# Kernel tuning notes

Hardware: AMD Instinct MI355X
Metric: run time of the kernel (lower is better)

## Reference

```python
import jax, jax.numpy as jnp
import numpy as np

B, L, S, D, H = 32, 256, 64, 128, 4
DH = D // H
EPS = 1e-5


def _uniform(k, shape, scale):
    return jax.random.uniform(k, shape, jnp.float32, -scale, scale)


def setup_inputs() -> dict:
    key = jax.random.key(0)
    ks = jax.random.split(key, 12)
    sc = 1.0 / np.sqrt(D)
    return {
        "h_wq": jax.random.normal(ks[0], (B, L, D), jnp.float32),
        "h_all": jax.random.normal(ks[1], (B, L, S, D), jnp.float32),
        "station_id": jax.random.randint(ks[2], (B,), 0, S),
        "adj": jax.random.randint(ks[3], (S, S), 0, 2).astype(jnp.float32),
        "in_proj_w": _uniform(ks[4], (3 * D, D), sc),
        "in_proj_b": _uniform(ks[5], (3 * D,), sc),
        "out_w": _uniform(ks[6], (D, D), sc),
        "out_b": _uniform(ks[7], (D,), sc),
        "gate_w": _uniform(ks[8], (D, 2 * D), 1.0 / np.sqrt(2 * D)),
        "gate_b": _uniform(ks[9], (D,), 1.0 / np.sqrt(2 * D)),
        "ln_g": jnp.ones((D,), jnp.float32),
        "ln_b": jnp.zeros((D,), jnp.float32),
        "alpha": jnp.asarray(0.1, jnp.float32),
    }


def _allowed_mask(adj, station_id):
    # allowed[b, s] == True  <=> station s may attend as key for sample b
    sid = station_id.astype(jnp.int32)
    allowed = adj[sid] > 0.0                                  # [B, S]
    self_oh = jax.nn.one_hot(sid, adj.shape[0], dtype=bool)   # [B, S]
    allowed = allowed & ~self_oh                              # exclude self
    # fallback-to-all for rows with no neighbor (still excluding self)
    no_nb = ~jnp.any(allowed, axis=1, keepdims=True)
    allowed = jnp.where(no_nb, ~self_oh, allowed)
    # final safety: if STILL empty (S==1 edge case), allow self
    no_nb2 = ~jnp.any(allowed, axis=1, keepdims=True)
    allowed = allowed | (no_nb2 & self_oh)
    return allowed


def _forward(h_wq, h_all, station_id, adj, in_proj_w, in_proj_b,
             out_w, out_b, gate_w, gate_b, ln_g, ln_b, alpha):
    b, l, d = h_wq.shape
    s = h_all.shape[2]
    qw, kw, vw = jnp.split(in_proj_w, 3, axis=0)
    qb, kb, vb = jnp.split(in_proj_b, 3, axis=0)

    q = (h_wq @ qw.T + qb).reshape(b, l, H, DH)        # [B,L,H,DH]
    k = (h_all @ kw.T + kb).reshape(b, l, s, H, DH)    # [B,L,S,H,DH]
    v = (h_all @ vw.T + vb).reshape(b, l, s, H, DH)

    scores = jnp.einsum('blhd,blshd->blhs', q, k) / np.sqrt(DH)  # [B,L,H,S]
    allowed = _allowed_mask(adj, station_id)                     # [B,S]
    scores = jnp.where(allowed[:, None, None, :], scores, -jnp.inf)
    w = jax.nn.softmax(scores, axis=-1)

    ctx = jnp.einsum('blhs,blshd->blhd', w, v).reshape(b, l, d)
    ctx = ctx @ out_w.T + out_b                                  # out_proj

    g = jax.nn.sigmoid(jnp.concatenate([h_wq, ctx], axis=-1) @ gate_w.T + gate_b)
    y = h_wq + alpha * (g * ctx)                                 # dropout = eval mode

    mu = jnp.mean(y, axis=-1, keepdims=True)
    var = jnp.mean(jnp.square(y - mu), axis=-1, keepdims=True)
    return (y - mu) * jax.lax.rsqrt(var + EPS) * ln_g + ln_b


def reference(h_wq, h_all, station_id, adj, in_proj_w, in_proj_b,
              out_w, out_b, gate_w, gate_b, ln_g, ln_b, alpha):
    return _forward(h_wq, h_all, station_id, adj, in_proj_w, in_proj_b,
                    out_w, out_b, gate_w, gate_b, ln_g, ln_b, alpha)
```

## Files before the change

### kernel.cpp

```cpp
#include <hip/hip_runtime.h>
#include <math.h>

#define B_   32
#define L_   256
#define S_   64
#define D_   128
#define H_   4
#define DH_  32
#define NTOK (B_*L_)

#define QK_OFF   0
#define QK_BYTES ((size_t)NTOK*512*4)
#define CB_OFF   (QK_OFF + QK_BYTES)
#define CB_BYTES ((size_t)NTOK*4*4)
#define CTX_OFF  (CB_OFF + CB_BYTES)

__global__ __launch_bounds__(256) void qk_kernel(
        const float* __restrict__ h_wq,
        const float* __restrict__ in_proj_w, const float* __restrict__ in_proj_b,
        float* __restrict__ qk_out, float* __restrict__ cb_out) {
    __shared__ float x_lds[32*128];
    __shared__ float q_lds[32*128];
    const int t0 = blockIdx.x * 32;
    const int tid = threadIdx.x;

    {
        const float4* src = (const float4*)(h_wq + (size_t)t0*128);
        float4* dst = (float4*)x_lds;
        for (int e = tid; e < 32*32; e += 256) dst[e] = src[e];
    }
    __syncthreads();

    const int d = tid & 127, half = tid >> 7;
    const float* xb = x_lds + half*16*128;
    {
        float acc[16];
        const float qb = in_proj_b[d];
        #pragma unroll
        for (int t = 0; t < 16; ++t) acc[t] = qb;
        const float4* wrow = (const float4*)(in_proj_w + (size_t)d*128);
        for (int j4 = 0; j4 < 32; ++j4) {
            float4 w = wrow[j4];
            #pragma unroll
            for (int t = 0; t < 16; ++t) {
                float4 x = *(const float4*)(xb + t*128 + j4*4);
                acc[t] += w.x*x.x + w.y*x.y + w.z*x.z + w.w*x.w;
            }
        }
        #pragma unroll
        for (int t = 0; t < 16; ++t) q_lds[(half*16+t)*128 + d] = acc[t];
    }
    __syncthreads();

    const float scale = 0.17677669529663687f;
    const float* qbse = q_lds + half*16*128;
    #pragma unroll
    for (int h = 0; h < 4; ++h) {
        float acc[16];
        #pragma unroll
        for (int t = 0; t < 16; ++t) acc[t] = 0.f;
        for (int j = 0; j < 32; ++j) {
            float w = in_proj_w[(size_t)(128 + h*32 + j)*128 + d];
            #pragma unroll
            for (int t = 0; t < 16; ++t) acc[t] += w * qbse[t*128 + h*32 + j];
        }
        #pragma unroll
        for (int t = 0; t < 16; ++t)
            qk_out[(size_t)(t0 + half*16 + t)*512 + h*128 + d] = acc[t] * scale;
    }
    if (tid < 128) {
        int t = tid >> 2, h = tid & 3;
        float s = 0.f;
        for (int j = 0; j < 32; ++j)
            s += q_lds[t*128 + h*32 + j] * in_proj_b[128 + h*32 + j];
        cb_out[(t0 + t)*4 + h] = s * scale;
    }
}

__global__ __launch_bounds__(256) void attn_kernel(
        const float* __restrict__ h_all,
        const float* __restrict__ in_proj_w, const float* __restrict__ in_proj_b,
        const float* __restrict__ qk_buf, const float* __restrict__ cb_buf,
        const int* __restrict__ station_id, const float* __restrict__ adj,
        float* __restrict__ ctx_out) {
    __shared__ float u_lds[4][4*132];
    __shared__ int   lst[64];
    __shared__ int   cnt_s;

    const int t0  = blockIdx.x * 4;
    const int b   = t0 >> 8;
    const int tid = threadIdx.x;
    const int wv  = tid >> 6;
    const int lane = tid & 63;
    const int g   = lane >> 4;
    const int lg  = lane & 15;
    const int t = t0 + wv;

    if (tid < 64) {
        int sid = station_id[b];
        int s = tid;
        bool av = (adj[sid*S_ + s] > 0.0f) && (s != sid);
        unsigned long long m = __ballot(av);
        if (m == 0ull) { av = (s != sid); m = __ballot(av); }
        if (m == 0ull) { av = (s == sid); m = __ballot(av); }
        int idx = __popcll(m & ((1ull << s) - 1ull));
        if (av) lst[idx] = s;
        if (s == 0) cnt_s = __popcll(m);
    }

    const float* qkp = qk_buf + (size_t)t*512 + g*128 + 8*lg;
    const float4 qa = *(const float4*)(qkp);
    const float4 qb = *(const float4*)(qkp + 4);
    const float cbg = cb_buf[t*4 + g];

    __syncthreads();
    const int cnt = cnt_s;
    const float* rowbase = h_all + (size_t)t * (S_*D_) + 8*lg;

    float mg = -INFINITY, lsum = 0.f;
    float4 ua = {0.f,0.f,0.f,0.f}, ub = {0.f,0.f,0.f,0.f};

    #pragma unroll 2
    for (int i = 0; i < cnt; ++i) {
        const float* rp = rowbase + lst[i]*D_;
        float4 xa = *(const float4*)(rp);
        float4 xb = *(const float4*)(rp + 4);
        float p = qa.x*xa.x + qa.y*xa.y + qa.z*xa.z + qa.w*xa.w
                + qb.x*xb.x + qb.y*xb.y + qb.z*xb.z + qb.w*xb.w;
        p += __shfl_xor(p, 8, 16);
        p += __shfl_xor(p, 4, 16);
        p += __shfl_xor(p, 2, 16);
        p += __shfl_xor(p, 1, 16);
        float s = p + cbg;
        float n = fmaxf(mg, s);
        float r = __expf(mg - n), w = __expf(s - n);
        lsum = lsum*r + w;
        ua.x = ua.x*r + w*xa.x; ua.y = ua.y*r + w*xa.y;
        ua.z = ua.z*r + w*xa.z; ua.w = ua.w*r + w*xa.w;
        ub.x = ub.x*r + w*xb.x; ub.y = ub.y*r + w*xb.y;
        ub.z = ub.z*r + w*xb.z; ub.w = ub.w*r + w*xb.w;
        mg = n;
    }
    {
        float inv = 1.f / lsum;
        ua.x *= inv; ua.y *= inv; ua.z *= inv; ua.w *= inv;
        ub.x *= inv; ub.y *= inv; ub.z *= inv; ub.w *= inv;
        *(float4*)&u_lds[wv][g*132 + 8*lg]     = ua;
        *(float4*)&u_lds[wv][g*132 + 8*lg + 4] = ub;
    }
    __syncthreads();

    {
        const int d = tid & 127, pr = tid >> 7, h = (tid & 127) >> 5;
        const float4* vwrow = (const float4*)(in_proj_w + (size_t)(256 + d)*128);
        const float vb = in_proj_b[256 + d];
        float a0 = vb, a1 = vb;
        const float* uA = &u_lds[2*pr][h*132];
        const float* uB = &u_lds[2*pr+1][h*132];
        #pragma unroll 8
        for (int j4 = 0; j4 < 32; ++j4) {
            float4 w = vwrow[j4];
            float4 v0 = *(const float4*)(uA + j4*4);
            float4 v1 = *(const float4*)(uB + j4*4);
            a0 += w.x*v0.x + w.y*v0.y + w.z*v0.z + w.w*v0.w;
            a1 += w.x*v1.x + w.y*v1.y + w.z*v1.z + w.w*v1.w;
        }
        ctx_out[(size_t)(t0 + 2*pr    )*128 + d] = a0;
        ctx_out[(size_t)(t0 + 2*pr + 1)*128 + d] = a1;
    }
}

__global__ __launch_bounds__(256) void epi_kernel(
        const float* __restrict__ h_wq, const float* __restrict__ ctx_buf,
        const float* __restrict__ out_w, const float* __restrict__ out_b,
        const float* __restrict__ gate_w, const float* __restrict__ gate_b,
        const float* __restrict__ ln_g, const float* __restrict__ ln_b,
        const float* __restrict__ alpha, float* __restrict__ out) {
    __shared__ float c_tile[32*128];
    __shared__ float x_tile[32*128];
    __shared__ float o_tile[32*128];
    __shared__ float mu_s[32], rs_s[32];
    const int t0 = blockIdx.x * 32;
    const int tid = threadIdx.x;

    {
        const float4* cs = (const float4*)(ctx_buf + (size_t)t0*128);
        const float4* xs = (const float4*)(h_wq + (size_t)t0*128);
        float4* cd = (float4*)c_tile; float4* xd = (float4*)x_tile;
        for (int e = tid; e < 32*32; e += 256) { cd[e] = cs[e]; xd[e] = xs[e]; }
    }
    __syncthreads();

    const int d = tid & 127, half = tid >> 7;
    float o_acc[16];
    {
        const float ob = out_b[d];
        #pragma unroll
        for (int t = 0; t < 16; ++t) o_acc[t] = ob;
        const float4* wrow = (const float4*)(out_w + (size_t)d*128);
        const float* cbp = c_tile + half*16*128;
        for (int j4 = 0; j4 < 32; ++j4) {
            float4 w = wrow[j4];
            #pragma unroll
            for (int t = 0; t < 16; ++t) {
                float4 c = *(const float4*)(cbp + t*128 + j4*4);
                o_acc[t] += w.x*c.x + w.y*c.y + w.z*c.z + w.w*c.w;
            }
        }
        #pragma unroll
        for (int t = 0; t < 16; ++t) o_tile[(half*16+t)*128 + d] = o_acc[t];
    }
    __syncthreads();

    {
        float g_acc[16];
        const float gb = gate_b[d];
        #pragma unroll
        for (int t = 0; t < 16; ++t) g_acc[t] = gb;
        const float4* wrow = (const float4*)(gate_w + (size_t)d*256);
        const float* xb = x_tile + half*16*128;
        const float* obp = o_tile + half*16*128;
        for (int j4 = 0; j4 < 32; ++j4) {
            float4 w0 = wrow[j4];
            float4 w1 = wrow[32 + j4];
            #pragma unroll
            for (int t = 0; t < 16; ++t) {
                float4 x = *(const float4*)(xb  + t*128 + j4*4);
                float4 o = *(const float4*)(obp + t*128 + j4*4);
                g_acc[t] += w0.x*x.x + w0.y*x.y + w0.z*x.z + w0.w*x.w
                          + w1.x*o.x + w1.y*o.y + w1.z*o.z + w1.w*o.w;
            }
        }
        const float al = alpha[0];
        #pragma unroll
        for (int t = 0; t < 16; ++t) {
            float g = 1.0f / (1.0f + __expf(-g_acc[t]));
            float y = xb[t*128 + d] + al * g * o_acc[t];
            c_tile[(half*16+t)*128 + d] = y;
        }
    }
    __syncthreads();

    {
        int tt = tid >> 3, k = tid & 7;
        const float* yr = c_tile + tt*128;
        float s = 0.f;
        for (int dd = k; dd < 128; dd += 8) s += yr[dd];
        for (int o = 4; o >= 1; o >>= 1) s += __shfl_xor(s, o, 8);
        float mu = s * (1.0f/128.0f);
        float vs = 0.f;
        for (int dd = k; dd < 128; dd += 8) { float df = yr[dd] - mu; vs += df*df; }
        for (int o = 4; o >= 1; o >>= 1) vs += __shfl_xor(vs, o, 8);
        if (k == 0) { mu_s[tt] = mu; rs_s[tt] = rsqrtf(vs*(1.0f/128.0f) + 1e-5f); }
    }
    __syncthreads();

    for (int e = tid; e < 32*128; e += 256) {
        int tt = e >> 7, dd = e & 127;
        float y = c_tile[e];
        out[(size_t)t0*128 + e] = (y - mu_s[tt]) * rs_s[tt] * ln_g[dd] + ln_b[dd];
    }
}

extern "C" void kernel_launch(void* const* d_in, const int* in_sizes, int n_in,
                              void* d_out, int out_size, void* d_ws, size_t ws_size,
                              hipStream_t stream) {
    const float* h_wq       = (const float*)d_in[0];
    const float* h_all      = (const float*)d_in[1];
    const int*   station_id = (const int*)  d_in[2];
    const float* adj        = (const float*)d_in[3];
    const float* in_proj_w  = (const float*)d_in[4];
    const float* in_proj_b  = (const float*)d_in[5];
    const float* out_w      = (const float*)d_in[6];
    const float* out_b      = (const float*)d_in[7];
    const float* gate_w     = (const float*)d_in[8];
    const float* gate_b     = (const float*)d_in[9];
    const float* ln_g       = (const float*)d_in[10];
    const float* ln_b       = (const float*)d_in[11];
    const float* alpha      = (const float*)d_in[12];

    char* ws = (char*)d_ws;
    float* qk   = (float*)(ws + QK_OFF);
    float* cb   = (float*)(ws + CB_OFF);
    float* ctx  = (float*)(ws + CTX_OFF);
    float* out  = (float*)d_out;

    qk_kernel  <<<NTOK/32, 256, 0, stream>>>(h_wq, in_proj_w, in_proj_b, qk, cb);
    attn_kernel<<<NTOK/4, 256, 0, stream>>>(h_all, in_proj_w, in_proj_b, qk, cb,
                                            station_id, adj, ctx);
    epi_kernel <<<NTOK/32, 256, 0, stream>>>(h_wq, ctx, out_w, out_b, gate_w,
                                             gate_b, ln_g, ln_b, alpha, out);
}
```

Baseline: 466.3 us.

## Fuse Q/K projection, attention and epilogue into one 4-token kernel

Merges the three kernels into a single kernel that processes 4 tokens per block. The q/k-folded projection, online-softmax attention, V projection, out projection, gate and layernorm all run in LDS, so the qk, cb and ctx workspace round-trips through global memory go away. The attention loop is also unrolled by hand to process two keys per step with a single max/rescale. In exchange each block now re-reads the in_proj, out and gate weights from cache for only 4 tokens instead of 32, which adds weight traffic and block-level syncs.

Measured after the change: 495.1 us. 1.06x slower.

```diff
diff --git a/kernel.cpp b/kernel.cpp
--- a/kernel.cpp
+++ b/kernel.cpp
@@ -5,96 +5,30 @@
 #define L_   256
 #define S_   64
 #define D_   128
-#define H_   4
-#define DH_  32
 #define NTOK (B_*L_)
 
-#define QK_OFF   0
-#define QK_BYTES ((size_t)NTOK*512*4)
-#define CB_OFF   (QK_OFF + QK_BYTES)
-#define CB_BYTES ((size_t)NTOK*4*4)
-#define CTX_OFF  (CB_OFF + CB_BYTES)
-
-__global__ __launch_bounds__(256) void qk_kernel(
-        const float* __restrict__ h_wq,
+__global__ __launch_bounds__(256) void fused_kernel(
+        const float* __restrict__ h_wq,  const float* __restrict__ h_all,
+        const int* __restrict__ station_id, const float* __restrict__ adj,
         const float* __restrict__ in_proj_w, const float* __restrict__ in_proj_b,
-        float* __restrict__ qk_out, float* __restrict__ cb_out) {
-    __shared__ float x_lds[32*128];
-    __shared__ float q_lds[32*128];
-    const int t0 = blockIdx.x * 32;
-    const int tid = threadIdx.x;
-
-    {
-        const float4* src = (const float4*)(h_wq + (size_t)t0*128);
-        float4* dst = (float4*)x_lds;
-        for (int e = tid; e < 32*32; e += 256) dst[e] = src[e];
-    }
-    __syncthreads();
-
-    const int d = tid & 127, half = tid >> 7;
-    const float* xb = x_lds + half*16*128;
-    {
-        float acc[16];
-        const float qb = in_proj_b[d];
-        #pragma unroll
-        for (int t = 0; t < 16; ++t) acc[t] = qb;
-        const float4* wrow = (const float4*)(in_proj_w + (size_t)d*128);
-        for (int j4 = 0; j4 < 32; ++j4) {
-            float4 w = wrow[j4];
-            #pragma unroll
-            for (int t = 0; t < 16; ++t) {
-                float4 x = *(const float4*)(xb + t*128 + j4*4);
-                acc[t] += w.x*x.x + w.y*x.y + w.z*x.z + w.w*x.w;
-            }
-        }
-        #pragma unroll
-        for (int t = 0; t < 16; ++t) q_lds[(half*16+t)*128 + d] = acc[t];
-    }
-    __syncthreads();
-
-    const float scale = 0.17677669529663687f;
-    const float* qbse = q_lds + half*16*128;
-    #pragma unroll
-    for (int h = 0; h < 4; ++h) {
-        float acc[16];
-        #pragma unroll
-        for (int t = 0; t < 16; ++t) acc[t] = 0.f;
-        for (int j = 0; j < 32; ++j) {
-            float w = in_proj_w[(size_t)(128 + h*32 + j)*128 + d];
-            #pragma unroll
-            for (int t = 0; t < 16; ++t) acc[t] += w * qbse[t*128 + h*32 + j];
-        }
-        #pragma unroll
-        for (int t = 0; t < 16; ++t)
-            qk_out[(size_t)(t0 + half*16 + t)*512 + h*128 + d] = acc[t] * scale;
-    }
-    if (tid < 128) {
-        int t = tid >> 2, h = tid & 3;
-        float s = 0.f;
-        for (int j = 0; j < 32; ++j)
-            s += q_lds[t*128 + h*32 + j] * in_proj_b[128 + h*32 + j];
-        cb_out[(t0 + t)*4 + h] = s * scale;
-    }
-}
-
-__global__ __launch_bounds__(256) void attn_kernel(
-        const float* __restrict__ h_all,
-        const float* __restrict__ in_proj_w, const float* __restrict__ in_proj_b,
-        const float* __restrict__ qk_buf, const float* __restrict__ cb_buf,
-        const int* __restrict__ station_id, const float* __restrict__ adj,
-        float* __restrict__ ctx_out) {
-    __shared__ float u_lds[4][4*132];
+        const float* __restrict__ out_w,  const float* __restrict__ out_b,
+        const float* __restrict__ gate_w, const float* __restrict__ gate_b,
+        const float* __restrict__ ln_g,   const float* __restrict__ ln_b,
+        const float* __restrict__ alpha,  float* __restrict__ out) {
+    __shared__ float X[4*132];
+    __shared__ float QK[4*528];
+    __shared__ float A[4*528];
+    __shared__ float cb[4][4];
     __shared__ int   lst[64];
     __shared__ int   cnt_s;
 
     const int t0  = blockIdx.x * 4;
     const int b   = t0 >> 8;
     const int tid = threadIdx.x;
-    const int wv  = tid >> 6;
-    const int lane = tid & 63;
-    const int g   = lane >> 4;
-    const int lg  = lane & 15;
-    const int t = t0 + wv;
+    const int wv  = tid >> 6, lane = tid & 63;
+    const int d   = tid & 127, pr = tid >> 7;
+    const int tA  = 2*pr, tB = 2*pr + 1;
+    const float scale = 0.17677669529663687f;
 
     if (tid < 64) {
         int sid = station_id[b];
@@ -107,158 +41,209 @@
         if (av) lst[idx] = s;
         if (s == 0) cnt_s = __popcll(m);
     }
-
-    const float* qkp = qk_buf + (size_t)t*512 + g*128 + 8*lg;
-    const float4 qa = *(const float4*)(qkp);
-    const float4 qb = *(const float4*)(qkp + 4);
-    const float cbg = cb_buf[t*4 + g];
-
-    __syncthreads();
-    const int cnt = cnt_s;
-    const float* rowbase = h_all + (size_t)t * (S_*D_) + 8*lg;
-
-    float mg = -INFINITY, lsum = 0.f;
-    float4 ua = {0.f,0.f,0.f,0.f}, ub = {0.f,0.f,0.f,0.f};
-
-    #pragma unroll 2
-    for (int i = 0; i < cnt; ++i) {
-        const float* rp = rowbase + lst[i]*D_;
-        float4 xa = *(const float4*)(rp);
-        float4 xb = *(const float4*)(rp + 4);
-        float p = qa.x*xa.x + qa.y*xa.y + qa.z*xa.z + qa.w*xa.w
-                + qb.x*xb.x + qb.y*xb.y + qb.z*xb.z + qb.w*xb.w;
-        p += __shfl_xor(p, 8, 16);
-        p += __shfl_xor(p, 4, 16);
-        p += __shfl_xor(p, 2, 16);
-        p += __shfl_xor(p, 1, 16);
-        float s = p + cbg;
-        float n = fmaxf(mg, s);
-        float r = __expf(mg - n), w = __expf(s - n);
-        lsum = lsum*r + w;
-        ua.x = ua.x*r + w*xa.x; ua.y = ua.y*r + w*xa.y;
-        ua.z = ua.z*r + w*xa.z; ua.w = ua.w*r + w*xa.w;
-        ub.x = ub.x*r + w*xb.x; ub.y = ub.y*r + w*xb.y;
-        ub.z = ub.z*r + w*xb.z; ub.w = ub.w*r + w*xb.w;
-        mg = n;
-    }
-    {
-        float inv = 1.f / lsum;
+    if (tid < 128) {
+        int tok = tid >> 5, d4 = tid & 31;
+        *(float4*)&X[tok*132 + d4*4] =
+            *(const float4*)(h_wq + (size_t)(t0 + tok)*128 + d4*4);
+    }
+    __syncthreads();
+
+    {
+        const float4* wrow = (const float4*)(in_proj_w + (size_t)d*128);
+        const float qb = in_proj_b[d];
+        float a0 = qb, a1 = qb;
+        const float* x0 = &X[tA*132];
+        const float* x1 = &X[tB*132];
+        #pragma unroll 8
+        for (int j4 = 0; j4 < 32; ++j4) {
+            float4 w  = wrow[j4];
+            float4 u0 = *(const float4*)(x0 + j4*4);
+            float4 u1 = *(const float4*)(x1 + j4*4);
+            a0 += w.x*u0.x + w.y*u0.y + w.z*u0.z + w.w*u0.w;
+            a1 += w.x*u1.x + w.y*u1.y + w.z*u1.z + w.w*u1.w;
+        }
+        A[tA*132 + d] = a0;
+        A[tB*132 + d] = a1;
+    }
+    __syncthreads();
+
+    {
+        const float* q0 = &A[tA*132];
+        const float* q1 = &A[tB*132];
+        #pragma unroll
+        for (int h = 0; h < 4; ++h) {
+            float a0 = 0.f, a1 = 0.f;
+            const float* wcol = in_proj_w + (size_t)(128 + h*32)*128 + d;
+            #pragma unroll 8
+            for (int j = 0; j < 32; ++j) {
+                float w = wcol[(size_t)j*128];
+                a0 += w * q0[h*32 + j];
+                a1 += w * q1[h*32 + j];
+            }
+            QK[tA*528 + h*132 + d] = a0 * scale;
+            QK[tB*528 + h*132 + d] = a1 * scale;
+        }
+    }
+    if (tid < 16) {
+        int tok = tid >> 2, h = tid & 3;
+        float s = 0.f;
+        for (int j = 0; j < 32; ++j)
+            s += A[tok*132 + h*32 + j] * in_proj_b[128 + h*32 + j];
+        cb[tok][h] = s * scale;
+    }
+    __syncthreads();
+
+    {
+        const int g = lane >> 4, lg = lane & 15;
+        const float4 qa  = *(const float4*)&QK[wv*528 + g*132 + 8*lg];
+        const float4 qb2 = *(const float4*)&QK[wv*528 + g*132 + 8*lg + 4];
+        const float cbg = cb[wv][g];
+        const int cnt = cnt_s;
+        const float* rowbase = h_all + (size_t)(t0 + wv)*(S_*D_) + 8*lg;
+
+        float mg = -INFINITY, ls = 0.f;
+        float4 ua = {0,0,0,0}, ub = {0,0,0,0};
+        int i = 0;
+        for (; i + 2 <= cnt; i += 2) {
+            const float* rp0 = rowbase + lst[i]*D_;
+            const float* rp1 = rowbase + lst[i+1]*D_;
+            float4 xa0 = *(const float4*)rp0, xb0 = *(const float4*)(rp0 + 4);
+            float4 xa1 = *(const float4*)rp1, xb1 = *(const float4*)(rp1 + 4);
+            float p0 = qa.x*xa0.x + qa.y*xa0.y + qa.z*xa0.z + qa.w*xa0.w
+                     + qb2.x*xb0.x + qb2.y*xb0.y + qb2.z*xb0.z + qb2.w*xb0.w;
+            float p1 = qa.x*xa1.x + qa.y*xa1.y + qa.z*xa1.z + qa.w*xa1.w
+                     + qb2.x*xb1.x + qb2.y*xb1.y + qb2.z*xb1.z + qb2.w*xb1.w;
+            p0 += __shfl_xor(p0, 8, 16);  p1 += __shfl_xor(p1, 8, 16);
+            p0 += __shfl_xor(p0, 4, 16);  p1 += __shfl_xor(p1, 4, 16);
+            p0 += __shfl_xor(p0, 2, 16);  p1 += __shfl_xor(p1, 2, 16);
+            p0 += __shfl_xor(p0, 1, 16);  p1 += __shfl_xor(p1, 1, 16);
+            float s0 = p0 + cbg, s1 = p1 + cbg;
+            float n = fmaxf(mg, fmaxf(s0, s1));
+            float r  = __expf(mg - n);
+            float w0 = __expf(s0 - n);
+            float w1 = __expf(s1 - n);
+            ls = ls*r + w0 + w1;
+            ua.x = ua.x*r + w0*xa0.x + w1*xa1.x;
+            ua.y = ua.y*r + w0*xa0.y + w1*xa1.y;
+            ua.z = ua.z*r + w0*xa0.z + w1*xa1.z;
+            ua.w = ua.w*r + w0*xa0.w + w1*xa1.w;
+            ub.x = ub.x*r + w0*xb0.x + w1*xb1.x;
+            ub.y = ub.y*r + w0*xb0.y + w1*xb1.y;
+            ub.z = ub.z*r + w0*xb0.z + w1*xb1.z;
+            ub.w = ub.w*r + w0*xb0.w + w1*xb1.w;
+            mg = n;
+        }
+        if (i < cnt) {
+            const float* rp0 = rowbase + lst[i]*D_;
+            float4 xa0 = *(const float4*)rp0, xb0 = *(const float4*)(rp0 + 4);
+            float p0 = qa.x*xa0.x + qa.y*xa0.y + qa.z*xa0.z + qa.w*xa0.w
+                     + qb2.x*xb0.x + qb2.y*xb0.y + qb2.z*xb0.z + qb2.w*xb0.w;
+            p0 += __shfl_xor(p0, 8, 16);
+            p0 += __shfl_xor(p0, 4, 16);
+            p0 += __shfl_xor(p0, 2, 16);
+            p0 += __shfl_xor(p0, 1, 16);
+            float s0 = p0 + cbg;
+            float n = fmaxf(mg, s0);
+            float r = __expf(mg - n), w0 = __expf(s0 - n);
+            ls = ls*r + w0;
+            ua.x = ua.x*r + w0*xa0.x; ua.y = ua.y*r + w0*xa0.y;
+            ua.z = ua.z*r + w0*xa0.z; ua.w = ua.w*r + w0*xa0.w;
+            ub.x = ub.x*r + w0*xb0.x; ub.y = ub.y*r + w0*xb0.y;
+            ub.z = ub.z*r + w0*xb0.z; ub.w = ub.w*r + w0*xb0.w;
+        }
+        float inv = 1.f / ls;
         ua.x *= inv; ua.y *= inv; ua.z *= inv; ua.w *= inv;
         ub.x *= inv; ub.y *= inv; ub.z *= inv; ub.w *= inv;
-        *(float4*)&u_lds[wv][g*132 + 8*lg]     = ua;
-        *(float4*)&u_lds[wv][g*132 + 8*lg + 4] = ub;
-    }
-    __syncthreads();
-
-    {
-        const int d = tid & 127, pr = tid >> 7, h = (tid & 127) >> 5;
+    __syncthreads();
+        *(float4*)&A[wv*528 + g*132 + 8*lg]     = ua;
+        *(float4*)&A[wv*528 + g*132 + 8*lg + 4] = ub;
+    }
+    __syncthreads();
+
+    {
+        const int h = d >> 5;
         const float4* vwrow = (const float4*)(in_proj_w + (size_t)(256 + d)*128);
         const float vb = in_proj_b[256 + d];
         float a0 = vb, a1 = vb;
-        const float* uA = &u_lds[2*pr][h*132];
-        const float* uB = &u_lds[2*pr+1][h*132];
+        const float* u0 = &A[tA*528 + h*132];
+        const float* u1 = &A[tB*528 + h*132];
         #pragma unroll 8
         for (int j4 = 0; j4 < 32; ++j4) {
-            float4 w = vwrow[j4];
-            float4 v0 = *(const float4*)(uA + j4*4);
-            float4 v1 = *(const float4*)(uB + j4*4);
+            float4 w  = vwrow[j4];
+            float4 v0 = *(const float4*)(u0 + j4*4);
+            float4 v1 = *(const float4*)(u1 + j4*4);
             a0 += w.x*v0.x + w.y*v0.y + w.z*v0.z + w.w*v0.w;
             a1 += w.x*v1.x + w.y*v1.y + w.z*v1.z + w.w*v1.w;
         }
-        ctx_out[(size_t)(t0 + 2*pr    )*128 + d] = a0;
-        ctx_out[(size_t)(t0 + 2*pr + 1)*128 + d] = a1;
-    }
-}
-
-__global__ __launch_bounds__(256) void epi_kernel(
-        const float* __restrict__ h_wq, const float* __restrict__ ctx_buf,
-        const float* __restrict__ out_w, const float* __restrict__ out_b,
-        const float* __restrict__ gate_w, const float* __restrict__ gate_b,
-        const float* __restrict__ ln_g, const float* __restrict__ ln_b,
-        const float* __restrict__ alpha, float* __restrict__ out) {
-    __shared__ float c_tile[32*128];
-    __shared__ float x_tile[32*128];
-    __shared__ float o_tile[32*128];
-    __shared__ float mu_s[32], rs_s[32];
-    const int t0 = blockIdx.x * 32;
-    const int tid = threadIdx.x;
-
-    {
-        const float4* cs = (const float4*)(ctx_buf + (size_t)t0*128);
-        const float4* xs = (const float4*)(h_wq + (size_t)t0*128);
-        float4* cd = (float4*)c_tile; float4* xd = (float4*)x_tile;
-        for (int e = tid; e < 32*32; e += 256) { cd[e] = cs[e]; xd[e] = xs[e]; }
-    }
-    __syncthreads();
-
-    const int d = tid & 127, half = tid >> 7;
-    float o_acc[16];
-    {
+        __syncthreads();
+        QK[tA*132 + d] = a0;
+        QK[tB*132 + d] = a1;
+    }
+    __syncthreads();
+
+    {
+        const float4* wrow = (const float4*)(out_w + (size_t)d*128);
         const float ob = out_b[d];
+        float a0 = ob, a1 = ob;
+        const float* c0 = &QK[tA*132];
+        const float* c1 = &QK[tB*132];
+        #pragma unroll 8
+        for (int j4 = 0; j4 < 32; ++j4) {
+            float4 w  = wrow[j4];
+            float4 v0 = *(const float4*)(c0 + j4*4);
+            float4 v1 = *(const float4*)(c1 + j4*4);
+            a0 += w.x*v0.x + w.y*v0.y + w.z*v0.z + w.w*v0.w;
+            a1 += w.x*v1.x + w.y*v1.y + w.z*v1.z + w.w*v1.w;
+        }
+        __syncthreads();
+        A[tA*132 + d] = a0;
+        A[tB*132 + d] = a1;
+    }
+    __syncthreads();
+
+    {
+        const float4* wrow = (const float4*)(gate_w + (size_t)d*256);
+        const float gb = gate_b[d];
+        float g0 = gb, g1 = gb;
+        const float* x0 = &X[tA*132];
+        const float* x1 = &X[tB*132];
+        const float* o0 = &A[tA*132];
+        const float* o1 = &A[tB*132];
+        #pragma unroll 4
+        for (int j4 = 0; j4 < 32; ++j4) {
+            float4 wx = wrow[j4];
+            float4 wo = wrow[32 + j4];
+            float4 vx0 = *(const float4*)(x0 + j4*4);
+            float4 vx1 = *(const float4*)(x1 + j4*4);
+            float4 vo0 = *(const float4*)(o0 + j4*4);
+            float4 vo1 = *(const float4*)(o1 + j4*4);
+            g0 += wx.x*vx0.x + wx.y*vx0.y + wx.z*vx0.z + wx.w*vx0.w
+                + wo.x*vo0.x + wo.y*vo0.y + wo.z*vo0.z + wo.w*vo0.w;
+            g1 += wx.x*vx1.x + wx.y*vx1.y + wx.z*vx1.z + wx.w*vx1.w
+                + wo.x*vo1.x + wo.y*vo1.y + wo.z*vo1.z + wo.w*vo1.w;
+        }
+        const float al = alpha[0];
+        float s0 = 1.0f / (1.0f + __expf(-g0));
+        float s1 = 1.0f / (1.0f + __expf(-g1));
+        QK[528 + tA*132 + d] = x0[d] + al * s0 * o0[d];
+        QK[528 + tB*132 + d] = x1[d] + al * s1 * o1[d];
+    }
+    __syncthreads();
+
+    {
+        float y0 = QK[528 + wv*132 + lane];
+        float y1 = QK[528 + wv*132 + 64 + lane];
+        float s = y0 + y1;
         #pragma unroll
-        for (int t = 0; t < 16; ++t) o_acc[t] = ob;
-        const float4* wrow = (const float4*)(out_w + (size_t)d*128);
-        const float* cbp = c_tile + half*16*128;
-        for (int j4 = 0; j4 < 32; ++j4) {
-            float4 w = wrow[j4];
-            #pragma unroll
-            for (int t = 0; t < 16; ++t) {
-                float4 c = *(const float4*)(cbp + t*128 + j4*4);
-                o_acc[t] += w.x*c.x + w.y*c.y + w.z*c.z + w.w*c.w;
-            }
-        }
+        for (int o = 32; o >= 1; o >>= 1) s += __shfl_xor(s, o);
+        float mu = s * (1.0f/128.0f);
+        float d0 = y0 - mu, d1 = y1 - mu;
+        float v = d0*d0 + d1*d1;
         #pragma unroll
-        for (int t = 0; t < 16; ++t) o_tile[(half*16+t)*128 + d] = o_acc[t];
-    }
-    __syncthreads();
-
-    {
-        float g_acc[16];
-        const float gb = gate_b[d];
-        #pragma unroll
-        for (int t = 0; t < 16; ++t) g_acc[t] = gb;
-        const float4* wrow = (const float4*)(gate_w + (size_t)d*256);
-        const float* xb = x_tile + half*16*128;
-        const float* obp = o_tile + half*16*128;
-        for (int j4 = 0; j4 < 32; ++j4) {
-            float4 w0 = wrow[j4];
-            float4 w1 = wrow[32 + j4];
-            #pragma unroll
-            for (int t = 0; t < 16; ++t) {
-                float4 x = *(const float4*)(xb  + t*128 + j4*4);
-                float4 o = *(const float4*)(obp + t*128 + j4*4);
-                g_acc[t] += w0.x*x.x + w0.y*x.y + w0.z*x.z + w0.w*x.w
-                          + w1.x*o.x + w1.y*o.y + w1.z*o.z + w1.w*o.w;
-            }
-        }
-        const float al = alpha[0];
-        #pragma unroll
-        for (int t = 0; t < 16; ++t) {
-            float g = 1.0f / (1.0f + __expf(-g_acc[t]));
-            float y = xb[t*128 + d] + al * g * o_acc[t];
-            c_tile[(half*16+t)*128 + d] = y;
-        }
-    }
-    __syncthreads();
-
-    {
-        int tt = tid >> 3, k = tid & 7;
-        const float* yr = c_tile + tt*128;
-        float s = 0.f;
-        for (int dd = k; dd < 128; dd += 8) s += yr[dd];
-        for (int o = 4; o >= 1; o >>= 1) s += __shfl_xor(s, o, 8);
-        float mu = s * (1.0f/128.0f);
-        float vs = 0.f;
-        for (int dd = k; dd < 128; dd += 8) { float df = yr[dd] - mu; vs += df*df; }
-        for (int o = 4; o >= 1; o >>= 1) vs += __shfl_xor(vs, o, 8);
-        if (k == 0) { mu_s[tt] = mu; rs_s[tt] = rsqrtf(vs*(1.0f/128.0f) + 1e-5f); }
-    }
-    __syncthreads();
-
-    for (int e = tid; e < 32*128; e += 256) {
-        int tt = e >> 7, dd = e & 127;
-        float y = c_tile[e];
-        out[(size_t)t0*128 + e] = (y - mu_s[tt]) * rs_s[tt] * ln_g[dd] + ln_b[dd];
+        for (int o = 32; o >= 1; o >>= 1) v += __shfl_xor(v, o);
+        float rs = rsqrtf(v*(1.0f/128.0f) + 1e-5f);
+        out[(size_t)(t0 + wv)*128 + lane]      = d0*rs*ln_g[lane]    + ln_b[lane];
+        out[(size_t)(t0 + wv)*128 + 64 + lane] = d1*rs*ln_g[64+lane] + ln_b[64+lane];
     }
 }
 
@@ -278,16 +263,9 @@
     const float* ln_g       = (const float*)d_in[10];
     const float* ln_b       = (const float*)d_in[11];
     const float* alpha      = (const float*)d_in[12];
-
-    char* ws = (char*)d_ws;
-    float* qk   = (float*)(ws + QK_OFF);
-    float* cb   = (float*)(ws + CB_OFF);
-    float* ctx  = (float*)(ws + CTX_OFF);
-    float* out  = (float*)d_out;
-
-    qk_kernel  <<<NTOK/32, 256, 0, stream>>>(h_wq, in_proj_w, in_proj_b, qk, cb);
-    attn_kernel<<<NTOK/4, 256, 0, stream>>>(h_all, in_proj_w, in_proj_b, qk, cb,
-                                            station_id, adj, ctx);
-    epi_kernel <<<NTOK/32, 256, 0, stream>>>(h_wq, ctx, out_w, out_b, gate_w,
-                                             gate_b, ln_g, ln_b, alpha, out);
+    float* out = (float*)d_out;
+
+    fused_kernel<<<NTOK/4, 256, 0, stream>>>(
+        h_wq, h_all, station_id, adj, in_proj_w, in_proj_b,
+        out_w, out_b, gate_w, gate_b, ln_g, ln_b, alpha, out);
 }
```
